# Kernel tuning notes

Hardware: AMD Instinct MI355X
Metric: run time of the kernel (lower is better)

## Reference

```python
import jax, jax.numpy as jnp
import numpy as np

NUM_CAPSULE = 10
DIM_CAPSULE = 16
ROUTINGS = 3
EPS = 1e-7  # K.epsilon()


def squash(x, axis=-1):
    sq_norm = jnp.sum(jnp.square(x), axis=axis, keepdims=True) + EPS
    coeff = jnp.sqrt(sq_norm) / (1.0 + sq_norm)
    return coeff * x


def setup_inputs() -> dict:
    key = jax.random.key(0)
    k1, k2 = jax.random.split(key)
    B, I, Din = 64, 4096, 128
    u_vecs = jax.random.normal(k1, (B, I, Din), dtype=jnp.float32)
    # glorot-ish scale for the capsule kernel (flattened conv1d kernel of size 1)
    W = jax.random.normal(k2, (Din, NUM_CAPSULE * DIM_CAPSULE), dtype=jnp.float32) * 0.06
    return {"u_vecs": u_vecs, "W": W}


def reference(u_vecs, W):
    B, I, Din = u_vecs.shape
    N, D = NUM_CAPSULE, DIM_CAPSULE
    # conv1d with kernel size 1 == per-position matmul
    u_hat = jnp.einsum('bid,dk->bik', u_vecs, W)          # [B, I, N*D]
    u_hat = u_hat.reshape(B, I, N, D).transpose(0, 2, 1, 3)  # [B, N, I, D]

    b = jnp.zeros((B, N, I), dtype=u_hat.dtype)
    outputs = None
    for i in range(ROUTINGS):
        c = jax.nn.softmax(b, axis=1)                      # softmax over num_capsule
        s = jnp.einsum('bni,bnid->bnd', c, u_hat)          # weighted sum over input caps
        outputs = squash(s)                                # [B, N, D]
        if i < ROUTINGS - 1:
            b = jnp.einsum('bnd,bnid->bni', outputs, u_hat)  # agreement logits
    return outputs
```

## Files before the change

kernel.cpp:

```cpp
#include <hip/hip_runtime.h>
#include <hip/hip_bf16.h>
#include <math.h>

#define NCAP 10
#define DCAP 16
#define DIN  128
#define NPOS 4096
#define NB   64

typedef short short8 __attribute__((ext_vector_type(8)));
typedef float floatx4 __attribute__((ext_vector_type(4)));

__device__ inline float bflo(unsigned v) { return __uint_as_float(v << 16); }
__device__ inline float bfhi(unsigned v) { return __uint_as_float(v & 0xFFFF0000u); }
__device__ inline unsigned short f2bf(float f) {
    unsigned u = __float_as_uint(f);
    return (unsigned short)((u + 0x7FFFu + ((u >> 16) & 1u)) >> 16);
}


__global__ __launch_bounds__(256) void caps_sum(const float* __restrict__ u,
                                                float* __restrict__ partial) {
    const int b = blockIdx.x;
    const int chunk = blockIdx.y;
    const int t = threadIdx.x;
    const int v4 = t & 31;
    const int prow = t >> 5;
    const float4* up = (const float4*)u;
    const size_t posbase = (size_t)b * NPOS + chunk * 128;

    float4 acc = make_float4(0.f, 0.f, 0.f, 0.f);
    #pragma unroll 8
    for (int j = 0; j < 16; ++j) {
        const size_t idx = (posbase + prow + j * 8) * 32 + v4;
        float4 x = up[idx];
        acc.x += x.x; acc.y += x.y; acc.z += x.z; acc.w += x.w;
    }
    __shared__ float4 red[8][32];
    red[prow][v4] = acc;
    __syncthreads();
    if (t < 32) {
        float4 s = red[0][t];
        #pragma unroll
        for (int r = 1; r < 8; ++r) {
            s.x += red[r][t].x; s.y += red[r][t].y;
            s.z += red[r][t].z; s.w += red[r][t].w;
        }
        ((float4*)partial)[((size_t)(b * 32 + chunk)) * 32 + t] = s;
    }
}

template <int MODE>
__global__ __launch_bounds__(128) void caps_small(const float* __restrict__ src,
                                                  const float* __restrict__ W,
                                                  float* __restrict__ dst) {
    const int b = blockIdx.x / NCAP;
    const int n = blockIdx.x % NCAP;
    const int t = threadIdx.x;
    __shared__ float xv[DIN];
    __shared__ float vv[DCAP];

    float a = 0.f;
    if (MODE == 0) {
        #pragma unroll 8
        for (int c = 0; c < 32; ++c)
            a += src[(size_t)(b * 32 + c) * DIN + t];
    } else {
        #pragma unroll 8
        for (int c = 0; c < 32; ++c)
            a += src[((size_t)(b * 32 + c) * NCAP + n) * DIN + t];
    }
    xv[t] = a;
    __syncthreads();

    if (t < DCAP) {
        float sv = 0.f;
        for (int d = 0; d < DIN; ++d)
            sv = fmaf(xv[d], W[d * 160 + n * DCAP + t], sv);
        if (MODE == 0) sv *= 0.1f;
        float nq = sv * sv;
        #pragma unroll
        for (int mm = 8; mm >= 1; mm >>= 1) nq += __shfl_xor(nq, mm, 16);
        nq += 1e-7f;
        const float v = sv * sqrtf(nq) / (1.0f + nq);
        if (MODE == 2)
            dst[(size_t)(b * NCAP + n) * DCAP + t] = v;
        else
            vv[t] = v;
    }
    if (MODE != 2) {
        __syncthreads();
        float wd = 0.f;
        #pragma unroll
        for (int dd = 0; dd < DCAP; ++dd)
            wd = fmaf(W[t * 160 + n * DCAP + dd], vv[dd], wd);
        dst[(size_t)(b * NCAP + n) * DIN + t] = wd;
    }
}

__global__ __launch_bounds__(256) void route_fx(const float* __restrict__ u,
                                                const float* __restrict__ wbuf,
                                                float* __restrict__ pws) {
    const int b = blockIdx.x;
    const int g = blockIdx.y;
    const int t = threadIdx.x;
    const int l = t & 63;
    const int w = __builtin_amdgcn_readfirstlane(t >> 6);

    __shared__ __align__(16) char smem[20480 + 64 * 12 * 4];
    uint4* tile = (uint4*)smem;
    float (*csm)[12] = (float (*)[12])(smem + 20480);

    const int an = l & 15;
    short8 af[4];
    #pragma unroll
    for (int kk = 0; kk < 4; ++kk) {
        short8 a = {0, 0, 0, 0, 0, 0, 0, 0};
        if (an < 10) {
            const float* wb = wbuf + ((size_t)(b * 10 + an)) * 128 +
                              (kk * 4 + (l >> 4)) * 8;
            const float4 x0 = *(const float4*)wb;
            const float4 x1 = *(const float4*)(wb + 4);
            a[0] = (short)f2bf(x0.x); a[1] = (short)f2bf(x0.y);
            a[2] = (short)f2bf(x0.z); a[3] = (short)f2bf(x0.w);
            a[4] = (short)f2bf(x1.x); a[5] = (short)f2bf(x1.y);
            a[6] = (short)f2bf(x1.z); a[7] = (short)f2bf(x1.w);
        }
        af[kk] = a;
    }

    const int d2 = t & 63;
    float acc[NCAP][2];
    #pragma unroll
    for (int n = 0; n < NCAP; ++n) { acc[n][0] = 0.f; acc[n][1] = 0.f; }

    for (int s = 0; s < 2; ++s) {
        __syncthreads();
        const float4* src4 = (const float4*)u +
            ((size_t)b * NPOS + g * 128 + s * 64) * 32;
        #pragma unroll
        for (int i = 0; i < 4; ++i) {
            const int q = t + i * 256;
            const int r = q >> 4, c = q & 15;
            const float4 x0 = src4[r * 32 + c * 2];
            const float4 x1 = src4[r * 32 + c * 2 + 1];
            uint4 h;
            h.x = (unsigned)f2bf(x0.x) | ((unsigned)f2bf(x0.y) << 16);
            h.y = (unsigned)f2bf(x0.z) | ((unsigned)f2bf(x0.w) << 16);
            h.z = (unsigned)f2bf(x1.x) | ((unsigned)f2bf(x1.y) << 16);
            h.w = (unsigned)f2bf(x1.z) | ((unsigned)f2bf(x1.w) << 16);
            tile[r * 16 + (c ^ (r & 7))] = h;
        }
        __syncthreads();

        floatx4 lg = {0.f, 0.f, 0.f, 0.f};
        #pragma unroll
        for (int kk = 0; kk < 4; ++kk) {
            const int br = w * 16 + (l & 15);
            const int q = kk * 4 + (l >> 4);
            const short8 bf = *(const short8*)&tile[br * 16 + (q ^ (br & 7))];
            lg = __builtin_amdgcn_mfma_f32_16x16x32_bf16(af[kk], bf, lg, 0, 0, 0);
        }

        const int ng = (l >> 4) * 4;
        float m = -1e30f;
        #pragma unroll
        for (int r2 = 0; r2 < 4; ++r2)
            if (ng + r2 < 10) m = fmaxf(m, lg[r2]);
        m = fmaxf(m, __shfl_xor(m, 16));
        m = fmaxf(m, __shfl_xor(m, 32));
        float e[4];
        float ss = 0.f;
        #pragma unroll
        for (int r2 = 0; r2 < 4; ++r2) {
            e[r2] = (ng + r2 < 10) ? __expf(lg[r2] - m) : 0.f;
            ss += e[r2];
        }
        ss += __shfl_xor(ss, 16);
        ss += __shfl_xor(ss, 32);
        const float inv = 1.0f / ss;
        const int posl = w * 16 + (l & 15);
        #pragma unroll
        for (int r2 = 0; r2 < 4; ++r2)
            if (ng + r2 < 10) csm[posl][ng + r2] = e[r2] * inv;
        __syncthreads();

        const unsigned* tlu = (const unsigned*)tile;
        #pragma unroll 4
        for (int i = 0; i < 16; ++i) {
            const int p = w * 16 + i;
            const unsigned v = tlu[(p * 16 + ((d2 >> 2) ^ (p & 7))) * 4 + (d2 & 3)];
            const float f0 = bflo(v), f1 = bfhi(v);
            const float4 c03 = *(const float4*)&csm[p][0];
            const float4 c47 = *(const float4*)&csm[p][4];
            const float2 c89 = *(const float2*)&csm[p][8];
            acc[0][0] = fmaf(c03.x, f0, acc[0][0]); acc[0][1] = fmaf(c03.x, f1, acc[0][1]);
            acc[1][0] = fmaf(c03.y, f0, acc[1][0]); acc[1][1] = fmaf(c03.y, f1, acc[1][1]);
            acc[2][0] = fmaf(c03.z, f0, acc[2][0]); acc[2][1] = fmaf(c03.z, f1, acc[2][1]);
            acc[3][0] = fmaf(c03.w, f0, acc[3][0]); acc[3][1] = fmaf(c03.w, f1, acc[3][1]);
            acc[4][0] = fmaf(c47.x, f0, acc[4][0]); acc[4][1] = fmaf(c47.x, f1, acc[4][1]);
            acc[5][0] = fmaf(c47.y, f0, acc[5][0]); acc[5][1] = fmaf(c47.y, f1, acc[5][1]);
            acc[6][0] = fmaf(c47.z, f0, acc[6][0]); acc[6][1] = fmaf(c47.z, f1, acc[6][1]);
            acc[7][0] = fmaf(c47.w, f0, acc[7][0]); acc[7][1] = fmaf(c47.w, f1, acc[7][1]);
            acc[8][0] = fmaf(c89.x, f0, acc[8][0]); acc[8][1] = fmaf(c89.x, f1, acc[8][1]);
            acc[9][0] = fmaf(c89.y, f0, acc[9][0]); acc[9][1] = fmaf(c89.y, f1, acc[9][1]);
        }
    }

    __syncthreads();
    float* red = (float*)smem;
    #pragma unroll
    for (int n = 0; n < NCAP; ++n) {
        red[w * 1280 + n * 128 + d2 * 2]     = acc[n][0];
        red[w * 1280 + n * 128 + d2 * 2 + 1] = acc[n][1];
    }
    __syncthreads();
    float* pb = pws + (size_t)(b * 32 + g) * 1280;
    #pragma unroll
    for (int o = 0; o < 5; ++o) {
        const int k = o * 256 + t;
        pb[k] = red[k] + red[1280 + k] + red[2560 + k] + red[3840 + k];
    }
}

extern "C" void kernel_launch(void* const* d_in, const int* in_sizes, int n_in,
                              void* d_out, int out_size, void* d_ws, size_t ws_size,
                              hipStream_t stream) {
    const float* u = (const float*)d_in[0];
    const float* W = (const float*)d_in[1];
    float* out = (float*)d_out;
    char* wsb = (char*)d_ws;

    float* partial = (float*)wsb;
    float* wbuf    = (float*)(wsb + 1048576);
    float* pws     = (float*)(wsb + 1376256);

    caps_sum<<<dim3(NB, 32), 256, 0, stream>>>(u, partial);
    caps_small<0><<<NB * NCAP, 128, 0, stream>>>(partial, W, wbuf);
    route_fx<<<dim3(NB, 32), 256, 0, stream>>>(u, wbuf, pws);
    caps_small<1><<<NB * NCAP, 128, 0, stream>>>(pws, W, wbuf);
    route_fx<<<dim3(NB, 32), 256, 0, stream>>>(u, wbuf, pws);
    caps_small<2><<<NB * NCAP, 128, 0, stream>>>(pws, W, out);
}
```

Baseline: 109.8 us.

## Fuse small squash/projection kernels into routing kernel prologue

Folds the per-(batch,capsule) partial reduction, squash and W-projection steps into the start of each routing kernel, so every routing block recomputes its batch's projected weights in shared memory. This drops two kernel launches and the global round trip through the intermediate weight buffer. In exchange, each of the 32 blocks per batch redundantly re-reduces the partials and re-does the small matmuls against W, which adds prologue latency and extra reads from the L2 cache. A second partial buffer is used so the two routing passes do not overwrite each other's inputs.

```diff
diff --git a/kernel.cpp b/kernel.cpp
--- a/kernel.cpp
+++ b/kernel.cpp
@@ -50,66 +50,69 @@
     }
 }
 
-template <int MODE>
-__global__ __launch_bounds__(128) void caps_small(const float* __restrict__ src,
-                                                  const float* __restrict__ W,
-                                                  float* __restrict__ dst) {
-    const int b = blockIdx.x / NCAP;
-    const int n = blockIdx.x % NCAP;
-    const int t = threadIdx.x;
-    __shared__ float xv[DIN];
-    __shared__ float vv[DCAP];
-
-    float a = 0.f;
-    if (MODE == 0) {
-        #pragma unroll 8
-        for (int c = 0; c < 32; ++c)
-            a += src[(size_t)(b * 32 + c) * DIN + t];
-    } else {
-        #pragma unroll 8
-        for (int c = 0; c < 32; ++c)
-            a += src[((size_t)(b * 32 + c) * NCAP + n) * DIN + t];
-    }
-    xv[t] = a;
-    __syncthreads();
-
-    if (t < DCAP) {
-        float sv = 0.f;
-        for (int d = 0; d < DIN; ++d)
-            sv = fmaf(xv[d], W[d * 160 + n * DCAP + t], sv);
-        if (MODE == 0) sv *= 0.1f;
-        float nq = sv * sv;
-        #pragma unroll
-        for (int mm = 8; mm >= 1; mm >>= 1) nq += __shfl_xor(nq, mm, 16);
-        nq += 1e-7f;
-        const float v = sv * sqrtf(nq) / (1.0f + nq);
-        if (MODE == 2)
-            dst[(size_t)(b * NCAP + n) * DCAP + t] = v;
-        else
-            vv[t] = v;
-    }
-    if (MODE != 2) {
-        __syncthreads();
-        float wd = 0.f;
-        #pragma unroll
-        for (int dd = 0; dd < DCAP; ++dd)
-            wd = fmaf(W[t * 160 + n * DCAP + dd], vv[dd], wd);
-        dst[(size_t)(b * NCAP + n) * DIN + t] = wd;
-    }
-}
-
-__global__ __launch_bounds__(256) void route_fx(const float* __restrict__ u,
-                                                const float* __restrict__ wbuf,
-                                                float* __restrict__ pws) {
+template <int SRC>
+__global__ __launch_bounds__(256) void route_fused(const float* __restrict__ u,
+                                                   const float* __restrict__ src,
+                                                   const float* __restrict__ W,
+                                                   float* __restrict__ pdst) {
     const int b = blockIdx.x;
     const int g = blockIdx.y;
     const int t = threadIdx.x;
     const int l = t & 63;
     const int w = __builtin_amdgcn_readfirstlane(t >> 6);
 
-    __shared__ __align__(16) char smem[20480 + 64 * 12 * 4];
+    __shared__ __align__(16) char smem[23552];
     uint4* tile = (uint4*)smem;
-    float (*csm)[12] = (float (*)[12])(smem + 20480);
+    float (*csm)[12] = (float (*)[12])(smem + 16384);
+    float* xvf  = (float*)smem;
+    float* wlds = (float*)(smem + 5120);
+    float* vv   = (float*)(smem + 10240);
+
+    if (SRC == 0) {
+        if (t < 128) {
+            float a = 0.f;
+            #pragma unroll 8
+            for (int c = 0; c < 32; ++c)
+                a += src[(size_t)(b * 32 + c) * DIN + t];
+            xvf[t] = a;
+        }
+    } else {
+        #pragma unroll
+        for (int o = 0; o < 5; ++o) {
+            const int k = o * 256 + t;
+            float a = 0.f;
+            #pragma unroll 8
+            for (int c = 0; c < 32; ++c)
+                a += src[(size_t)(b * 32 + c) * 1280 + k];
+            xvf[k] = a;
+        }
+    }
+    __syncthreads();
+    if (t < 160) {
+        const int n = t >> 4, j = t & 15;
+        const float* xb = (SRC == 0) ? xvf : (xvf + n * 128);
+        float sv = 0.f;
+        for (int d = 0; d < DIN; ++d)
+            sv = fmaf(xb[d], W[d * 160 + n * DCAP + j], sv);
+        if (SRC == 0) sv *= 0.1f;
+        float nq = sv * sv;
+        #pragma unroll
+        for (int mm = 8; mm >= 1; mm >>= 1) nq += __shfl_xor(nq, mm, 16);
+        nq += 1e-7f;
+        vv[t] = sv * sqrtf(nq) / (1.0f + nq);
+    }
+    __syncthreads();
+    #pragma unroll
+    for (int o = 0; o < 5; ++o) {
+        const int k = o * 256 + t;
+        const int n = k >> 7, d = k & 127;
+        float wd = 0.f;
+        #pragma unroll
+        for (int j = 0; j < DCAP; ++j)
+            wd = fmaf(W[d * 160 + n * DCAP + j], vv[n * DCAP + j], wd);
+        wlds[k] = wd;
+    }
+    __syncthreads();
 
     const int an = l & 15;
     short8 af[4];
@@ -117,8 +120,7 @@
     for (int kk = 0; kk < 4; ++kk) {
         short8 a = {0, 0, 0, 0, 0, 0, 0, 0};
         if (an < 10) {
-            const float* wb = wbuf + ((size_t)(b * 10 + an)) * 128 +
-                              (kk * 4 + (l >> 4)) * 8;
+            const float* wb = wlds + an * 128 + (kk * 4 + (l >> 4)) * 8;
             const float4 x0 = *(const float4*)wb;
             const float4 x1 = *(const float4*)(wb + 4);
             a[0] = (short)f2bf(x0.x); a[1] = (short)f2bf(x0.y);
@@ -215,11 +217,38 @@
         red[w * 1280 + n * 128 + d2 * 2 + 1] = acc[n][1];
     }
     __syncthreads();
-    float* pb = pws + (size_t)(b * 32 + g) * 1280;
+    float* pb = pdst + (size_t)(b * 32 + g) * 1280;
     #pragma unroll
     for (int o = 0; o < 5; ++o) {
         const int k = o * 256 + t;
         pb[k] = red[k] + red[1280 + k] + red[2560 + k] + red[3840 + k];
+    }
+}
+
+__global__ __launch_bounds__(128) void small_out(const float* __restrict__ src,
+                                                 const float* __restrict__ W,
+                                                 float* __restrict__ out) {
+    const int b = blockIdx.x / NCAP;
+    const int n = blockIdx.x % NCAP;
+    const int t = threadIdx.x;
+    __shared__ float xv[DIN];
+
+    float a = 0.f;
+    #pragma unroll 8
+    for (int c = 0; c < 32; ++c)
+        a += src[((size_t)(b * 32 + c) * NCAP + n) * DIN + t];
+    xv[t] = a;
+    __syncthreads();
+
+    if (t < DCAP) {
+        float sv = 0.f;
+        for (int d = 0; d < DIN; ++d)
+            sv = fmaf(xv[d], W[d * 160 + n * DCAP + t], sv);
+        float nq = sv * sv;
+        #pragma unroll
+        for (int mm = 8; mm >= 1; mm >>= 1) nq += __shfl_xor(nq, mm, 16);
+        nq += 1e-7f;
+        out[(size_t)(b * NCAP + n) * DCAP + t] = sv * sqrtf(nq) / (1.0f + nq);
     }
 }
 
@@ -232,13 +261,11 @@
     char* wsb = (char*)d_ws;
 
     float* partial = (float*)wsb;
-    float* wbuf    = (float*)(wsb + 1048576);
-    float* pws     = (float*)(wsb + 1376256);
+    float* pws     = (float*)(wsb + 1048576);
+    float* pws2    = (float*)(wsb + 11534336);
 
     caps_sum<<<dim3(NB, 32), 256, 0, stream>>>(u, partial);
-    caps_small<0><<<NB * NCAP, 128, 0, stream>>>(partial, W, wbuf);
-    route_fx<<<dim3(NB, 32), 256, 0, stream>>>(u, wbuf, pws);
-    caps_small<1><<<NB * NCAP, 128, 0, stream>>>(pws, W, wbuf);
-    route_fx<<<dim3(NB, 32), 256, 0, stream>>>(u, wbuf, pws);
-    caps_small<2><<<NB * NCAP, 128, 0, stream>>>(pws, W, out);
-}
+    route_fused<0><<<dim3(NB, 32), 256, 0, stream>>>(u, partial, W, pws);
+    route_fused<1><<<dim3(NB, 32), 256, 0, stream>>>(u, pws, W, pws2);
+    small_out<<<NB * NCAP, 128, 0, stream>>>(pws2, W, out);
+}
```

New measurement: 149.2 us. +35.9%, slower.
